# Kernel tuning notes

Hardware: AMD Instinct MI355X
Metric: run time of the kernel (lower is better)

## Reference

```python
import jax, jax.numpy as jnp
import numpy as np

WS = (8, 8)       # window size (wh, ww)
SS = (4, 4)       # shift size
NUM_HEADS = 8


def _relative_position_index(wh, ww):
    coords = np.stack(np.meshgrid(np.arange(wh), np.arange(ww), indexing='ij'))  # [2,wh,ww]
    cf = coords.reshape(2, -1)                                # [2, N]
    rel = (cf[:, :, None] - cf[:, None, :]).transpose(1, 2, 0)  # [N,N,2]
    rel[..., 0] += wh - 1
    rel[..., 1] += ww - 1
    rel[..., 0] *= 2 * ww - 1
    return rel.sum(-1).reshape(-1)                            # [N*N]


def _shift_attn_mask(H, W, wh, ww, sh, sw):
    img = np.zeros((H, W), dtype=np.float32)
    cnt = 0
    for hs in ((0, -wh), (-wh, -sh), (-sh, None)):
        for ws_ in ((0, -ww), (-ww, -sw), (-sw, None)):
            img[hs[0]:hs[1], ws_[0]:ws_[1]] = cnt
            cnt += 1
    m = img.reshape(H // wh, wh, W // ww, ww).transpose(0, 2, 1, 3).reshape(-1, wh * ww)  # [nW, N]
    diff = m[:, None, :] - m[:, :, None]                      # [nW, N, N]
    return np.where(diff != 0, -100.0, 0.0).astype(np.float32)


def setup_inputs() -> dict:
    key = jax.random.key(0)
    ks = jax.random.split(key, 6)
    B, H, W, C = 16, 128, 128, 256
    return {
        'x': jax.random.normal(ks[0], (B, H, W, C), jnp.float32),
        'qkv_weight': jax.random.normal(ks[1], (3 * C, C), jnp.float32) * 0.02,
        'qkv_bias': jax.random.normal(ks[2], (3 * C,), jnp.float32) * 0.02,
        'proj_weight': jax.random.normal(ks[3], (C, C), jnp.float32) * 0.02,
        'proj_bias': jax.random.normal(ks[4], (C,), jnp.float32) * 0.02,
        'rel_bias_table': jax.random.normal(ks[5], ((2 * WS[0] - 1) * (2 * WS[1] - 1), NUM_HEADS), jnp.float32) * 0.02,
    }


def reference(x, qkv_weight, qkv_bias, proj_weight, proj_bias, rel_bias_table):
    B, H, W, C = x.shape
    wh, ww = WS
    sh, sw = SS
    nh = NUM_HEADS
    hd = C // nh
    N = wh * ww
    nW = (H // wh) * (W // ww)

    # relative position bias [1, nh, N, N]
    rpi = _relative_position_index(wh, ww)
    bias = rel_bias_table[rpi].reshape(N, N, nh).transpose(2, 0, 1)[None]

    # shift (H, W divisible by window -> no padding needed)
    xs = jnp.roll(x, shift=(-sh, -sw), axis=(1, 2))
    # window partition -> [B*nW, N, C]
    xw = xs.reshape(B, H // wh, wh, W // ww, ww, C).transpose(0, 1, 3, 2, 4, 5).reshape(B * nW, N, C)

    qkv = xw @ qkv_weight.T + qkv_bias                        # [BnW, N, 3C]
    qkv = qkv.reshape(B * nW, N, 3, nh, hd).transpose(2, 0, 3, 1, 4)
    q, k, v = qkv[0], qkv[1], qkv[2]                          # [BnW, nh, N, hd]
    q = q * (hd ** -0.5)

    attn = jnp.einsum('whnd,whmd->whnm', q, k) + bias         # [BnW, nh, N, N]
    if sh + sw > 0:
        mask = jnp.asarray(_shift_attn_mask(H, W, wh, ww, sh, sw))  # [nW, N, N]
        attn = attn.reshape(B, nW, nh, N, N) + mask[None, :, None]
        attn = attn.reshape(B * nW, nh, N, N)
    attn = jax.nn.softmax(attn, axis=-1)

    out = jnp.einsum('whnm,whmd->whnd', attn, v)              # [BnW, nh, N, hd]
    out = out.transpose(0, 2, 1, 3).reshape(B * nW, N, C)
    out = out @ proj_weight.T + proj_bias

    # window reverse
    out = out.reshape(B, H // wh, W // ww, wh, ww, C).transpose(0, 1, 3, 2, 4, 5).reshape(B, H, W, C)
    out = jnp.roll(out, shift=(sh, sw), axis=(1, 2))
    return out
```

## Files before the change

### kernel.cpp

```cpp
#include <hip/hip_runtime.h>


typedef float f32x4 __attribute__((ext_vector_type(4)));
typedef __bf16 bf16x8 __attribute__((ext_vector_type(8)));
typedef unsigned short u16x4 __attribute__((ext_vector_type(4)));
typedef unsigned short u16x8 __attribute__((ext_vector_type(8)));

#define MFMA16(a, b, c) __builtin_amdgcn_mfma_f32_16x16x32_bf16((a), (b), (c), 0, 0, 0)

__device__ __forceinline__ unsigned short f2bf(float f) {
  union { float f; unsigned u; } v; v.f = f;
  unsigned r = v.u + 0x7FFFu + ((v.u >> 16) & 1u);
  return (unsigned short)(r >> 16);
}

__device__ __forceinline__ bf16x8 pack8(float4 f0, float4 f1) {
  union { u16x8 s; bf16x8 v; } u;
  u.s[0] = f2bf(f0.x); u.s[1] = f2bf(f0.y); u.s[2] = f2bf(f0.z); u.s[3] = f2bf(f0.w);
  u.s[4] = f2bf(f1.x); u.s[5] = f2bf(f1.y); u.s[6] = f2bf(f1.z); u.s[7] = f2bf(f1.w);
  return u.v;
}

__device__ __forceinline__ bf16x8 ld8u(const unsigned short* p) {
  union { unsigned long long q[2]; bf16x8 v; } u;
  u.q[0] = *(const unsigned long long*)(p);
  u.q[1] = *(const unsigned long long*)(p + 4);
  return u.v;
}

#define Q_OFF   0
#define K_OFF   18432
#define V_OFF   36864
#define TAB_OFF 55296
#define P_OFF   58912
#define SM_TOT  77344

__global__ void conv_weights(const float* __restrict__ qkvW, const float* __restrict__ projW,
                             unsigned short* __restrict__ wq, unsigned short* __restrict__ wp) {
  int i = blockIdx.x * 256 + threadIdx.x;
  if (i < 196608) wq[i] = f2bf(qkvW[i]);
  if (i < 65536)  wp[i] = f2bf(projW[i]);
}

template <bool PRE>
__global__ __launch_bounds__(256, 1) void swin_fused(
    const float* __restrict__ x,
    const float* __restrict__ qkvWf,
    const float* __restrict__ qkvB,
    const float* __restrict__ projWf,
    const float* __restrict__ projB,
    const float* __restrict__ relTab,
    const unsigned short* __restrict__ qkvWb,
    const unsigned short* __restrict__ projWb,
    float* __restrict__ out) {
  __shared__ unsigned short sm[SM_TOT];
  const f32x4 Z = {0.0f, 0.0f, 0.0f, 0.0f};

  const int tid = threadIdx.x;
  const int wv  = tid >> 6;
  const int lane = tid & 63;
  const int g  = lane >> 4;
  const int cl = lane & 15;
  const int blk = blockIdx.x;
  const int b  = blk >> 8;
  const int w  = blk & 255;
  const int wi = w >> 4, wj = w & 15;
  const bool er = (wi == 15), ec = (wj == 15);

  {
    float* t = (float*)(sm + TAB_OFF);
    for (int i = tid; i < 1800; i += 256) t[i] = relTab[i];
  }
  {
    unsigned short* X = sm + P_OFF;
    const float* xb = x + (size_t)b * (128 * 128 * 256);
#pragma unroll
    for (int it = 0; it < 8; ++it) {
      int idx = tid + it * 256;
      int t = idx >> 5, ch = idx & 31;
      int hh = (wi * 8 + (t >> 3) + 4) & 127;
      int ww = (wj * 8 + (t & 7) + 4) & 127;
      const float* src = xb + (((hh << 7) + ww) << 8) + ch * 8;
      float4 f0 = *(const float4*)src;
      float4 f1 = *(const float4*)(src + 4);
      u16x8 pk;
      pk[0] = f2bf(f0.x); pk[1] = f2bf(f0.y); pk[2] = f2bf(f0.z); pk[3] = f2bf(f0.w);
      pk[4] = f2bf(f1.x); pk[5] = f2bf(f1.y); pk[6] = f2bf(f1.z); pk[7] = f2bf(f1.w);
      *(u16x8*)(X + t * 256 + ((ch ^ (t & 7)) << 3)) = pk;
    }
  }
  __syncthreads();

  {
    const unsigned short* X = sm + P_OFF;
    for (int ct = wv * 12; ct < wv * 12 + 12; ++ct) {
      const int cb = ct << 4;
      bf16x8 bw[8];
#pragma unroll
      for (int ks = 0; ks < 8; ++ks) {
        const int off = (cb + cl) * 256 + ks * 32 + g * 8;
        if (PRE) {
          bw[ks] = *(const bf16x8*)(qkvWb + off);
        } else {
          float4 f0 = *(const float4*)(qkvWf + off);
          float4 f1 = *(const float4*)(qkvWf + off + 4);
          bw[ks] = pack8(f0, f1);
        }
      }
      f32x4 acc[4] = {Z, Z, Z, Z};
#pragma unroll
      for (int rt = 0; rt < 4; ++rt) {
        const int t = rt * 16 + cl;
        const unsigned short* xr = X + t * 256;
        const int t7 = t & 7;
#pragma unroll
        for (int ks = 0; ks < 8; ++ks) {
          bf16x8 a = *(const bf16x8*)(xr + (((ks * 4 + g) ^ t7) << 3));
          acc[rt] = MFMA16(a, bw[ks], acc[rt]);
        }
      }
      const int col = cb + cl;
      const float bias = qkvB[col];
      const int sel = col >> 8;
      const int hd_ = (col >> 5) & 7;
      const int dim = col & 31;
#pragma unroll
      for (int rt = 0; rt < 4; ++rt) {
#pragma unroll
        for (int rg = 0; rg < 4; ++rg) {
          const int t = rt * 16 + g * 4 + rg;
          float v = acc[rt][rg] + bias;
          if (sel == 0) {
            sm[Q_OFF + hd_ * 2304 + t * 36 + dim] = f2bf(v * 0.17677669529663687f);
          } else if (sel == 1) {
            sm[K_OFF + hd_ * 2304 + t * 36 + dim] = f2bf(v);
          } else {
            sm[V_OFF + (hd_ * 32 + dim) * 72 + t] = f2bf(v);
          }
        }
      }
    }
  }
  __syncthreads();

  {
    const float* tab = (const float*)(sm + TAB_OFF);
    unsigned short* P = sm + P_OFF + wv * 4608;
    float rsum[4];
#pragma unroll 1
    for (int hp = 0; hp < 2; ++hp) {
      const int h = wv * 2 + hp;
      const unsigned short* qh = sm + Q_OFF + h * 2304;
      const unsigned short* kh = sm + K_OFF + h * 2304;
      const unsigned short* vh = sm + V_OFF + h * (32 * 72);

      bf16x8 aq[4], ak[4];
#pragma unroll
      for (int qt = 0; qt < 4; ++qt) {
        aq[qt] = ld8u(qh + (qt * 16 + cl) * 36 + g * 8);
        ak[qt] = ld8u(kh + (qt * 16 + cl) * 36 + g * 8);
      }
      f32x4 s[4][4];
#pragma unroll
      for (int qt = 0; qt < 4; ++qt)
#pragma unroll
        for (int jt = 0; jt < 4; ++jt)
          s[qt][jt] = MFMA16(ak[jt], aq[qt], Z);

#pragma unroll
      for (int qt = 0; qt < 4; ++qt) {
        const int i = qt * 16 + cl;
        const int ri = i >> 3, ci = i & 7;
        const int ridi = (er ? ((ri < 4) ? 3 : 6) : 0) + (ec ? ((ci < 4) ? 1 : 2) : 0);
        float m = -1e30f;
#pragma unroll
        for (int jt = 0; jt < 4; ++jt) {
#pragma unroll
          for (int rg = 0; rg < 4; ++rg) {
            const int j = jt * 16 + g * 4 + rg;
            const int rj = j >> 3, cj = j & 7;
            const int ridj = (er ? ((rj < 4) ? 3 : 6) : 0) + (ec ? ((cj < 4) ? 1 : 2) : 0);
            float val = s[qt][jt][rg] + tab[((ri - rj + 7) * 15 + (ci - cj + 7)) * 8 + h];
            if (ridi != ridj) val -= 100.0f;
            s[qt][jt][rg] = val;
            m = fmaxf(m, val);
          }
        }
        m = fmaxf(m, __shfl_xor(m, 16));
        m = fmaxf(m, __shfl_xor(m, 32));
        float sum = 0.0f;
#pragma unroll
        for (int jt = 0; jt < 4; ++jt)
#pragma unroll
          for (int rg = 0; rg < 4; ++rg) {
            float e = __expf(s[qt][jt][rg] - m);
            s[qt][jt][rg] = e;
            sum += e;
          }
        sum += __shfl_xor(sum, 16);
        sum += __shfl_xor(sum, 32);
        rsum[qt] = 1.0f / sum;
      }

#pragma unroll
      for (int qt = 0; qt < 4; ++qt) {
        const int i = qt * 16 + cl;
#pragma unroll
        for (int jt = 0; jt < 4; ++jt) {
          u16x4 pk;
          pk[0] = f2bf(s[qt][jt][0]); pk[1] = f2bf(s[qt][jt][1]);
          pk[2] = f2bf(s[qt][jt][2]); pk[3] = f2bf(s[qt][jt][3]);
          *(u16x4*)(P + i * 72 + jt * 16 + g * 4) = pk;
        }
      }

      f32x4 o[2][4] = {{Z, Z, Z, Z}, {Z, Z, Z, Z}};
#pragma unroll
      for (int ks = 0; ks < 2; ++ks) {
        bf16x8 av[2], bp[4];
        av[0] = *(const bf16x8*)(vh + cl * 72 + ks * 32 + g * 8);
        av[1] = *(const bf16x8*)(vh + (16 + cl) * 72 + ks * 32 + g * 8);
#pragma unroll
        for (int qt = 0; qt < 4; ++qt)
          bp[qt] = *(const bf16x8*)(P + (qt * 16 + cl) * 72 + ks * 32 + g * 8);
#pragma unroll
        for (int dt = 0; dt < 2; ++dt)
#pragma unroll
          for (int qt = 0; qt < 4; ++qt)
            o[dt][qt] = MFMA16(av[dt], bp[qt], o[dt][qt]);
      }
#pragma unroll
      for (int dt = 0; dt < 2; ++dt)
#pragma unroll
        for (int qt = 0; qt < 4; ++qt) {
          u16x4 pk;
#pragma unroll
          for (int rg = 0; rg < 4; ++rg) pk[rg] = f2bf(o[dt][qt][rg] * rsum[qt]);
          const int t = qt * 16 + cl;
          *(u16x4*)(sm + Q_OFF + h * 2304 + t * 36 + dt * 16 + g * 4) = pk;
        }
    }
  }
  __syncthreads();

  {
    for (int ct = wv * 4; ct < wv * 4 + 4; ++ct) {
      const int cb = ct << 4;
      bf16x8 bw[8];
#pragma unroll
      for (int ks = 0; ks < 8; ++ks) {
        const int off = (cb + cl) * 256 + ks * 32 + g * 8;
        if (PRE) {
          bw[ks] = *(const bf16x8*)(projWb + off);
        } else {
          float4 f0 = *(const float4*)(projWf + off);
          float4 f1 = *(const float4*)(projWf + off + 4);
          bw[ks] = pack8(f0, f1);
        }
      }
      f32x4 acc[4] = {Z, Z, Z, Z};
#pragma unroll
      for (int rt = 0; rt < 4; ++rt) {
#pragma unroll
        for (int ks = 0; ks < 8; ++ks) {
          bf16x8 a = ld8u(sm + Q_OFF + ks * 2304 + (rt * 16 + cl) * 36 + g * 8);
          acc[rt] = MFMA16(a, bw[ks], acc[rt]);
        }
      }
      const int chn = cb + cl;
      const float pb = projB[chn];
#pragma unroll
      for (int rt = 0; rt < 4; ++rt) {
#pragma unroll
        for (int rg = 0; rg < 4; ++rg) {
          const int t = rt * 16 + g * 4 + rg;
          const int ho = (wi * 8 + (t >> 3) + 4) & 127;
          const int wo = (wj * 8 + (t & 7) + 4) & 127;
          out[((size_t)((b << 14) + (ho << 7) + wo) << 8) + chn] = acc[rt][rg] + pb;
        }
      }
    }
  }
}

extern "C" void kernel_launch(void* const* d_in, const int* in_sizes, int n_in,
                              void* d_out, int out_size, void* d_ws, size_t ws_size,
                              hipStream_t stream) {
  const float* x     = (const float*)d_in[0];
  const float* qkvW  = (const float*)d_in[1];
  const float* qkvB  = (const float*)d_in[2];
  const float* projW = (const float*)d_in[3];
  const float* projB = (const float*)d_in[4];
  const float* tab   = (const float*)d_in[5];
  float* out = (float*)d_out;

  const size_t need = (size_t)(196608 + 65536) * sizeof(unsigned short);
  if (ws_size >= need) {
    unsigned short* wq = (unsigned short*)d_ws;
    unsigned short* wp = wq + 196608;
    conv_weights<<<dim3(768), dim3(256), 0, stream>>>(qkvW, projW, wq, wp);
    swin_fused<true><<<dim3(4096), dim3(256), 0, stream>>>(
        x, qkvW, qkvB, projW, projB, tab, wq, wp, out);
  } else {
    swin_fused<false><<<dim3(4096), dim3(256), 0, stream>>>(
        x, qkvW, qkvB, projW, projB, tab, nullptr, nullptr, out);
  }
}
```

Measured before the change: 1.002 ms.

## Restructure fused Swin kernel per-head with smaller LDS and precomputed bias+mask

Each wave now computes Q, K and V for its own two heads and goes straight into attention from registers, using a small per-wave LDS scratch. This replaces the full-window Q/K/V staging in shared memory. LDS use drops from about 150KB to about 48KB, and launch bounds are raised to allow 3 blocks per CU. A prep kernel precomputes the relative-position bias plus shift mask for the four edge variants and folds the q scale into the bf16 qkv weights. The cost is more register pressure and a reworked, swizzled LDS layout, plus a global bias read per score tile.

```diff
diff --git a/kernel.cpp b/kernel.cpp
--- a/kernel.cpp
+++ b/kernel.cpp
@@ -7,6 +7,7 @@
 typedef unsigned short u16x8 __attribute__((ext_vector_type(8)));
 
 #define MFMA16(a, b, c) __builtin_amdgcn_mfma_f32_16x16x32_bf16((a), (b), (c), 0, 0, 0)
+#define QSCALE 0.17677669529663687f
 
 __device__ __forceinline__ unsigned short f2bf(float f) {
   union { float f; unsigned u; } v; v.f = f;
@@ -21,265 +22,294 @@
   return u.v;
 }
 
-__device__ __forceinline__ bf16x8 ld8u(const unsigned short* p) {
-  union { unsigned long long q[2]; bf16x8 v; } u;
-  u.q[0] = *(const unsigned long long*)(p);
-  u.q[1] = *(const unsigned long long*)(p + 4);
-  return u.v;
-}
-
-#define Q_OFF   0
-#define K_OFF   18432
-#define V_OFF   36864
-#define TAB_OFF 55296
-#define P_OFF   58912
-#define SM_TOT  77344
-
-__global__ void conv_weights(const float* __restrict__ qkvW, const float* __restrict__ projW,
-                             unsigned short* __restrict__ wq, unsigned short* __restrict__ wp) {
+__global__ void prep(const float* __restrict__ qkvW, const float* __restrict__ projW,
+                     const float* __restrict__ relTab,
+                     unsigned short* __restrict__ wq, unsigned short* __restrict__ wp,
+                     float* __restrict__ biasm) {
   int i = blockIdx.x * 256 + threadIdx.x;
-  if (i < 196608) wq[i] = f2bf(qkvW[i]);
-  if (i < 65536)  wp[i] = f2bf(projW[i]);
+  if (i < 196608) {
+    float v = qkvW[i];
+    if (i < 65536) v *= QSCALE;
+    wq[i] = f2bf(v);
+  }
+  if (i < 65536) wp[i] = f2bf(projW[i]);
+  if (i < 131072) {
+    int j = i & 63, ii = (i >> 6) & 63, h = (i >> 12) & 7, var = i >> 15;
+    int er = var >> 1, ec = var & 1;
+    int ri = ii >> 3, ci = ii & 7, rj = j >> 3, cj = j & 7;
+    int ridi = (er ? ((ri < 4) ? 3 : 6) : 0) + (ec ? ((ci < 4) ? 1 : 2) : 0);
+    int ridj = (er ? ((rj < 4) ? 3 : 6) : 0) + (ec ? ((cj < 4) ? 1 : 2) : 0);
+    float v = relTab[((ri - rj + 7) * 15 + (ci - cj + 7)) * 8 + h];
+    if (ridi != ridj) v -= 100.0f;
+    biasm[i] = v;
+  }
 }
 
 template <bool PRE>
-__global__ __launch_bounds__(256, 1) void swin_fused(
+__global__ __launch_bounds__(256, 3) void swin_fused(
     const float* __restrict__ x,
-    const float* __restrict__ qkvWf,
-    const float* __restrict__ qkvB,
-    const float* __restrict__ projWf,
-    const float* __restrict__ projB,
+    const float* __restrict__ qkvWf, const float* __restrict__ qkvB,
+    const float* __restrict__ projWf, const float* __restrict__ projB,
     const float* __restrict__ relTab,
     const unsigned short* __restrict__ qkvWb,
     const unsigned short* __restrict__ projWb,
+    const float* __restrict__ biasm,
     float* __restrict__ out) {
-  __shared__ unsigned short sm[SM_TOT];
+  __shared__ unsigned short sm[PRE ? 24576 : 28192];
   const f32x4 Z = {0.0f, 0.0f, 0.0f, 0.0f};
 
   const int tid = threadIdx.x;
-  const int wv  = tid >> 6;
-  const int lane = tid & 63;
-  const int g  = lane >> 4;
-  const int cl = lane & 15;
-  const int blk = blockIdx.x;
-  const int b  = blk >> 8;
-  const int w  = blk & 255;
-  const int wi = w >> 4, wj = w & 15;
+  const int wv = tid >> 6, lane = tid & 63, g = lane >> 4, cl = lane & 15;
+  const int blk = blockIdx.x, b = blk >> 8, w = blk & 255, wi = w >> 4, wj = w & 15;
   const bool er = (wi == 15), ec = (wj == 15);
+  const int var = (er ? 2 : 0) + (ec ? 1 : 0);
+
+  if (!PRE) {
+    float* t = (float*)(sm + 24576);
+    for (int i = tid; i < 1800; i += 256) t[i] = relTab[i];
+  }
 
   {
-    float* t = (float*)(sm + TAB_OFF);
-    for (int i = tid; i < 1800; i += 256) t[i] = relTab[i];
-  }
-  {
-    unsigned short* X = sm + P_OFF;
     const float* xb = x + (size_t)b * (128 * 128 * 256);
 #pragma unroll
     for (int it = 0; it < 8; ++it) {
-      int idx = tid + it * 256;
-      int t = idx >> 5, ch = idx & 31;
+      int idx = tid + it * 256, t = idx >> 5, ch = idx & 31;
       int hh = (wi * 8 + (t >> 3) + 4) & 127;
       int ww = (wj * 8 + (t & 7) + 4) & 127;
-      const float* src = xb + (((hh << 7) + ww) << 8) + ch * 8;
+      const float* src = xb + ((((hh << 7) + ww) << 8) + ch * 8);
       float4 f0 = *(const float4*)src;
       float4 f1 = *(const float4*)(src + 4);
-      u16x8 pk;
-      pk[0] = f2bf(f0.x); pk[1] = f2bf(f0.y); pk[2] = f2bf(f0.z); pk[3] = f2bf(f0.w);
-      pk[4] = f2bf(f1.x); pk[5] = f2bf(f1.y); pk[6] = f2bf(f1.z); pk[7] = f2bf(f1.w);
-      *(u16x8*)(X + t * 256 + ((ch ^ (t & 7)) << 3)) = pk;
+      union { u16x8 s; bf16x8 v; } pk;
+      pk.s[0] = f2bf(f0.x); pk.s[1] = f2bf(f0.y); pk.s[2] = f2bf(f0.z); pk.s[3] = f2bf(f0.w);
+      pk.s[4] = f2bf(f1.x); pk.s[5] = f2bf(f1.y); pk.s[6] = f2bf(f1.z); pk.s[7] = f2bf(f1.w);
+      *(u16x8*)(sm + ch * 512 + ((t ^ (2 * (ch & 3))) << 3)) = pk.s;
     }
   }
   __syncthreads();
 
-  {
-    const unsigned short* X = sm + P_OFF;
-    for (int ct = wv * 12; ct < wv * 12 + 12; ++ct) {
-      const int cb = ct << 4;
+  unsigned short* scr = sm + 16384 + wv * 2048;
+  const int hA = wv * 2, hB = hA + 1;
+
+  auto ldx = [&](int row, int c) -> bf16x8 {
+    return *(const bf16x8*)(sm + c * 512 + ((row ^ (2 * (c & 3))) << 3));
+  };
+  auto gemm32 = [&](int colbase, f32x4 (&acc)[2][4]) {
+#pragma unroll
+    for (int ct = 0; ct < 2; ++ct) {
+      const int col = colbase + ct * 16 + cl;
       bf16x8 bw[8];
 #pragma unroll
       for (int ks = 0; ks < 8; ++ks) {
-        const int off = (cb + cl) * 256 + ks * 32 + g * 8;
-        if (PRE) {
-          bw[ks] = *(const bf16x8*)(qkvWb + off);
-        } else {
-          float4 f0 = *(const float4*)(qkvWf + off);
-          float4 f1 = *(const float4*)(qkvWf + off + 4);
-          bw[ks] = pack8(f0, f1);
+        const int off = col * 256 + ks * 32 + g * 8;
+        if (PRE) bw[ks] = *(const bf16x8*)(qkvWb + off);
+        else {
+          float4 a = *(const float4*)(qkvWf + off);
+          float4 c2 = *(const float4*)(qkvWf + off + 4);
+          bw[ks] = pack8(a, c2);
         }
       }
-      f32x4 acc[4] = {Z, Z, Z, Z};
 #pragma unroll
       for (int rt = 0; rt < 4; ++rt) {
-        const int t = rt * 16 + cl;
-        const unsigned short* xr = X + t * 256;
-        const int t7 = t & 7;
-#pragma unroll
-        for (int ks = 0; ks < 8; ++ks) {
-          bf16x8 a = *(const bf16x8*)(xr + (((ks * 4 + g) ^ t7) << 3));
-          acc[rt] = MFMA16(a, bw[ks], acc[rt]);
+        acc[ct][rt] = Z;
+#pragma unroll
+        for (int ks = 0; ks < 8; ++ks)
+          acc[ct][rt] = MFMA16(ldx(rt * 16 + cl, ks * 4 + g), bw[ks], acc[ct][rt]);
+      }
+    }
+  };
+  auto epiQK = [&](f32x4 (&acc)[2][4], int colbase, bool isQ) {
+#pragma unroll
+    for (int ct = 0; ct < 2; ++ct) {
+      const int col = colbase + ct * 16 + cl;
+      float bs = qkvB[col]; if (isQ) bs *= QSCALE;
+      const int cQ = 2 * ct + (cl >> 3), Xr = 2 * (cQ & 3);
+#pragma unroll
+      for (int rt = 0; rt < 4; ++rt)
+#pragma unroll
+        for (int r = 0; r < 4; ++r) {
+          float v = acc[ct][rt][r];
+          if (!PRE && isQ) v *= QSCALE;
+          scr[cQ * 512 + (((rt * 16 + 4 * g + r) ^ Xr) << 3) + (cl & 7)] = f2bf(v + bs);
         }
-      }
-      const int col = cb + cl;
-      const float bias = qkvB[col];
-      const int sel = col >> 8;
-      const int hd_ = (col >> 5) & 7;
-      const int dim = col & 31;
+    }
+  };
+  auto ldQK = [&](int it) -> bf16x8 {
+    return *(const bf16x8*)(scr + g * 512 + (((it * 16 + cl) ^ (2 * g)) << 3));
+  };
+  auto epiV = [&](f32x4 (&acc)[2][4], int colbase) {
+#pragma unroll
+    for (int ct = 0; ct < 2; ++ct) {
+      const int col = colbase + ct * 16 + cl;
+      const float bs = qkvB[col];
 #pragma unroll
       for (int rt = 0; rt < 4; ++rt) {
-#pragma unroll
-        for (int rg = 0; rg < 4; ++rg) {
-          const int t = rt * 16 + g * 4 + rg;
-          float v = acc[rt][rg] + bias;
-          if (sel == 0) {
-            sm[Q_OFF + hd_ * 2304 + t * 36 + dim] = f2bf(v * 0.17677669529663687f);
-          } else if (sel == 1) {
-            sm[K_OFF + hd_ * 2304 + t * 36 + dim] = f2bf(v);
-          } else {
-            sm[V_OFF + (hd_ * 32 + dim) * 72 + t] = f2bf(v);
-          }
-        }
-      }
-    }
-  }
-  __syncthreads();
-
-  {
-    const float* tab = (const float*)(sm + TAB_OFF);
-    unsigned short* P = sm + P_OFF + wv * 4608;
-    float rsum[4];
-#pragma unroll 1
-    for (int hp = 0; hp < 2; ++hp) {
-      const int h = wv * 2 + hp;
-      const unsigned short* qh = sm + Q_OFF + h * 2304;
-      const unsigned short* kh = sm + K_OFF + h * 2304;
-      const unsigned short* vh = sm + V_OFF + h * (32 * 72);
-
-      bf16x8 aq[4], ak[4];
-#pragma unroll
-      for (int qt = 0; qt < 4; ++qt) {
-        aq[qt] = ld8u(qh + (qt * 16 + cl) * 36 + g * 8);
-        ak[qt] = ld8u(kh + (qt * 16 + cl) * 36 + g * 8);
-      }
-      f32x4 s[4][4];
-#pragma unroll
-      for (int qt = 0; qt < 4; ++qt)
-#pragma unroll
-        for (int jt = 0; jt < 4; ++jt)
-          s[qt][jt] = MFMA16(ak[jt], aq[qt], Z);
-
-#pragma unroll
-      for (int qt = 0; qt < 4; ++qt) {
-        const int i = qt * 16 + cl;
+        const int cV = 2 * rt + (g >> 1);
+        const int pos = (ct * 16 + cl) ^ (2 * (cV & 3));
+        u16x4 pk;
+#pragma unroll
+        for (int r = 0; r < 4; ++r) pk[r] = f2bf(acc[ct][rt][r] + bs);
+        *(u16x4*)(scr + cV * 256 + pos * 8 + 4 * (g & 1)) = pk;
+      }
+    }
+  };
+  auto ldV = [&](int ks, int dt) -> bf16x8 {
+    const int c = ks * 4 + g;
+    return *(const bf16x8*)(scr + c * 256 + (((dt * 16 + cl) ^ (2 * (c & 3))) << 3));
+  };
+  auto attnHead = [&](int h, bf16x8 (&aq)[4], bf16x8 (&ak)[4], bf16x8 (&bv)[2][2],
+                      f32x4 (&o)[4][2]) {
+    bf16x8 ap[4][2];
+#pragma unroll
+    for (int qt = 0; qt < 4; ++qt) {
+      f32x4 s4[4];
+#pragma unroll
+      for (int jt = 0; jt < 4; ++jt) s4[jt] = MFMA16(ak[jt], aq[qt], Z);
+      const int i = qt * 16 + cl;
+      if (PRE) {
+        const float* bp = biasm + (((var * 8 + h) * 64 + i) << 6) + g * 4;
+#pragma unroll
+        for (int jt = 0; jt < 4; ++jt) s4[jt] += *(const f32x4*)(bp + jt * 16);
+      } else {
+        const float* tab = (const float*)(sm + 24576);
         const int ri = i >> 3, ci = i & 7;
         const int ridi = (er ? ((ri < 4) ? 3 : 6) : 0) + (ec ? ((ci < 4) ? 1 : 2) : 0);
-        float m = -1e30f;
-#pragma unroll
-        for (int jt = 0; jt < 4; ++jt) {
-#pragma unroll
-          for (int rg = 0; rg < 4; ++rg) {
-            const int j = jt * 16 + g * 4 + rg;
-            const int rj = j >> 3, cj = j & 7;
+#pragma unroll
+        for (int jt = 0; jt < 4; ++jt)
+#pragma unroll
+          for (int r = 0; r < 4; ++r) {
+            const int j = jt * 16 + 4 * g + r, rj = j >> 3, cj = j & 7;
             const int ridj = (er ? ((rj < 4) ? 3 : 6) : 0) + (ec ? ((cj < 4) ? 1 : 2) : 0);
-            float val = s[qt][jt][rg] + tab[((ri - rj + 7) * 15 + (ci - cj + 7)) * 8 + h];
-            if (ridi != ridj) val -= 100.0f;
-            s[qt][jt][rg] = val;
-            m = fmaxf(m, val);
+            float v2 = s4[jt][r] + tab[((ri - rj + 7) * 15 + (ci - cj + 7)) * 8 + h];
+            if (ridi != ridj) v2 -= 100.0f;
+            s4[jt][r] = v2;
           }
+      }
+      float mx = -1e30f;
+#pragma unroll
+      for (int jt = 0; jt < 4; ++jt)
+#pragma unroll
+        for (int r = 0; r < 4; ++r) mx = fmaxf(mx, s4[jt][r]);
+      mx = fmaxf(mx, __shfl_xor(mx, 16));
+      mx = fmaxf(mx, __shfl_xor(mx, 32));
+      float sum = 0.0f;
+#pragma unroll
+      for (int jt = 0; jt < 4; ++jt)
+#pragma unroll
+        for (int r = 0; r < 4; ++r) {
+          float e = __expf(s4[jt][r] - mx);
+          s4[jt][r] = e; sum += e;
         }
-        m = fmaxf(m, __shfl_xor(m, 16));
-        m = fmaxf(m, __shfl_xor(m, 32));
-        float sum = 0.0f;
-#pragma unroll
-        for (int jt = 0; jt < 4; ++jt)
-#pragma unroll
-          for (int rg = 0; rg < 4; ++rg) {
-            float e = __expf(s[qt][jt][rg] - m);
-            s[qt][jt][rg] = e;
-            sum += e;
-          }
-        sum += __shfl_xor(sum, 16);
-        sum += __shfl_xor(sum, 32);
-        rsum[qt] = 1.0f / sum;
-      }
-
-#pragma unroll
-      for (int qt = 0; qt < 4; ++qt) {
-        const int i = qt * 16 + cl;
-#pragma unroll
-        for (int jt = 0; jt < 4; ++jt) {
-          u16x4 pk;
-          pk[0] = f2bf(s[qt][jt][0]); pk[1] = f2bf(s[qt][jt][1]);
-          pk[2] = f2bf(s[qt][jt][2]); pk[3] = f2bf(s[qt][jt][3]);
-          *(u16x4*)(P + i * 72 + jt * 16 + g * 4) = pk;
-        }
-      }
-
-      f32x4 o[2][4] = {{Z, Z, Z, Z}, {Z, Z, Z, Z}};
-#pragma unroll
-      for (int ks = 0; ks < 2; ++ks) {
-        bf16x8 av[2], bp[4];
-        av[0] = *(const bf16x8*)(vh + cl * 72 + ks * 32 + g * 8);
-        av[1] = *(const bf16x8*)(vh + (16 + cl) * 72 + ks * 32 + g * 8);
-#pragma unroll
-        for (int qt = 0; qt < 4; ++qt)
-          bp[qt] = *(const bf16x8*)(P + (qt * 16 + cl) * 72 + ks * 32 + g * 8);
-#pragma unroll
-        for (int dt = 0; dt < 2; ++dt)
-#pragma unroll
-          for (int qt = 0; qt < 4; ++qt)
-            o[dt][qt] = MFMA16(av[dt], bp[qt], o[dt][qt]);
-      }
-#pragma unroll
-      for (int dt = 0; dt < 2; ++dt)
-#pragma unroll
-        for (int qt = 0; qt < 4; ++qt) {
-          u16x4 pk;
-#pragma unroll
-          for (int rg = 0; rg < 4; ++rg) pk[rg] = f2bf(o[dt][qt][rg] * rsum[qt]);
-          const int t = qt * 16 + cl;
-          *(u16x4*)(sm + Q_OFF + h * 2304 + t * 36 + dt * 16 + g * 4) = pk;
-        }
-    }
+      sum += __shfl_xor(sum, 16);
+      sum += __shfl_xor(sum, 32);
+      const float rs = 1.0f / sum;
+#pragma unroll
+      for (int jt = 0; jt < 4; ++jt) {
+        const int cP = 2 * jt + (g >> 1);
+        const int pos = cl ^ (2 * (cP & 3));
+        u16x4 pk;
+#pragma unroll
+        for (int r = 0; r < 4; ++r) pk[r] = f2bf(s4[jt][r] * rs);
+        *(u16x4*)(scr + cP * 128 + pos * 8 + 4 * (g & 1)) = pk;
+      }
+#pragma unroll
+      for (int ks = 0; ks < 2; ++ks)
+        ap[qt][ks] = *(const bf16x8*)(scr + (ks * 4 + g) * 128 + ((cl ^ (2 * g)) << 3));
+    }
+#pragma unroll
+    for (int it = 0; it < 4; ++it)
+#pragma unroll
+      for (int dt = 0; dt < 2; ++dt) {
+        o[it][dt] = Z;
+#pragma unroll
+        for (int ks = 0; ks < 2; ++ks)
+          o[it][dt] = MFMA16(ap[it][ks], bv[ks][dt], o[it][dt]);
+      }
+  };
+  auto writeO = [&](int h, f32x4 (&o)[4][2]) {
+#pragma unroll
+    for (int it = 0; it < 4; ++it)
+#pragma unroll
+      for (int dt = 0; dt < 2; ++dt) {
+        const int d = h * 32 + dt * 16 + cl;
+        const int cA = d >> 3, Xr = 2 * (cA & 3);
+#pragma unroll
+        for (int r = 0; r < 4; ++r)
+          sm[cA * 512 + (((it * 16 + 4 * g + r) ^ Xr) << 3) + (d & 7)] = f2bf(o[it][dt][r]);
+      }
+  };
+
+  bf16x8 aqA[4], akA[4], bvA[2][2], aqB[4], akB[4], bvB[2][2];
+  {
+    f32x4 acc[2][4];
+    gemm32(hA * 32, acc);        epiQK(acc, hA * 32, true);
+#pragma unroll
+    for (int i2 = 0; i2 < 4; ++i2) aqA[i2] = ldQK(i2);
+    gemm32(256 + hA * 32, acc);  epiQK(acc, 256 + hA * 32, false);
+#pragma unroll
+    for (int i2 = 0; i2 < 4; ++i2) akA[i2] = ldQK(i2);
+    gemm32(512 + hA * 32, acc);  epiV(acc, 512 + hA * 32);
+#pragma unroll
+    for (int ks = 0; ks < 2; ++ks)
+#pragma unroll
+      for (int dt = 0; dt < 2; ++dt) bvA[ks][dt] = ldV(ks, dt);
+    gemm32(hB * 32, acc);        epiQK(acc, hB * 32, true);
+#pragma unroll
+    for (int i2 = 0; i2 < 4; ++i2) aqB[i2] = ldQK(i2);
+    gemm32(256 + hB * 32, acc);  epiQK(acc, 256 + hB * 32, false);
+#pragma unroll
+    for (int i2 = 0; i2 < 4; ++i2) akB[i2] = ldQK(i2);
+  }
+  f32x4 oA[4][2];
+  attnHead(hA, aqA, akA, bvA, oA);
+  {
+    f32x4 acc[2][4];
+    gemm32(512 + hB * 32, acc);  epiV(acc, 512 + hB * 32);
+#pragma unroll
+    for (int ks = 0; ks < 2; ++ks)
+#pragma unroll
+      for (int dt = 0; dt < 2; ++dt) bvB[ks][dt] = ldV(ks, dt);
   }
   __syncthreads();
-
+  writeO(hA, oA);
   {
-    for (int ct = wv * 4; ct < wv * 4 + 4; ++ct) {
-      const int cb = ct << 4;
-      bf16x8 bw[8];
-#pragma unroll
-      for (int ks = 0; ks < 8; ++ks) {
-        const int off = (cb + cl) * 256 + ks * 32 + g * 8;
-        if (PRE) {
-          bw[ks] = *(const bf16x8*)(projWb + off);
-        } else {
-          float4 f0 = *(const float4*)(projWf + off);
-          float4 f1 = *(const float4*)(projWf + off + 4);
-          bw[ks] = pack8(f0, f1);
-        }
-      }
-      f32x4 acc[4] = {Z, Z, Z, Z};
-#pragma unroll
-      for (int rt = 0; rt < 4; ++rt) {
-#pragma unroll
-        for (int ks = 0; ks < 8; ++ks) {
-          bf16x8 a = ld8u(sm + Q_OFF + ks * 2304 + (rt * 16 + cl) * 36 + g * 8);
-          acc[rt] = MFMA16(a, bw[ks], acc[rt]);
-        }
-      }
-      const int chn = cb + cl;
-      const float pb = projB[chn];
-#pragma unroll
-      for (int rt = 0; rt < 4; ++rt) {
-#pragma unroll
-        for (int rg = 0; rg < 4; ++rg) {
-          const int t = rt * 16 + g * 4 + rg;
-          const int ho = (wi * 8 + (t >> 3) + 4) & 127;
-          const int wo = (wj * 8 + (t & 7) + 4) & 127;
-          out[((size_t)((b << 14) + (ho << 7) + wo) << 8) + chn] = acc[rt][rg] + pb;
-        }
-      }
-    }
+    f32x4 oB[4][2];
+    attnHead(hB, aqB, akB, bvB, oB);
+    writeO(hB, oB);
+  }
+  __syncthreads();
+
+#pragma unroll 1
+  for (int ct = wv * 4; ct < wv * 4 + 4; ++ct) {
+    const int col = ct * 16 + cl;
+    bf16x8 bw[8];
+#pragma unroll
+    for (int ks = 0; ks < 8; ++ks) {
+      const int off = col * 256 + ks * 32 + g * 8;
+      if (PRE) bw[ks] = *(const bf16x8*)(projWb + off);
+      else {
+        float4 a = *(const float4*)(projWf + off);
+        float4 c2 = *(const float4*)(projWf + off + 4);
+        bw[ks] = pack8(a, c2);
+      }
+    }
+    f32x4 acc[4];
+#pragma unroll
+    for (int rt = 0; rt < 4; ++rt) {
+      acc[rt] = Z;
+#pragma unroll
+      for (int ks = 0; ks < 8; ++ks)
+        acc[rt] = MFMA16(ldx(rt * 16 + cl, ks * 4 + g), bw[ks], acc[rt]);
+    }
+    const float pb = projB[col];
+#pragma unroll
+    for (int rt = 0; rt < 4; ++rt)
+#pragma unroll
+      for (int r = 0; r < 4; ++r) {
+        const int t = rt * 16 + 4 * g + r;
+        const int ho = (wi * 8 + (t >> 3) + 4) & 127;
+        const int wo = (wj * 8 + (t & 7) + 4) & 127;
+        out[((size_t)((b << 14) + (ho << 7) + wo) << 8) + col] = acc[rt][r] + pb;
+      }
   }
 }
 
@@ -294,15 +324,17 @@
   const float* tab   = (const float*)d_in[5];
   float* out = (float*)d_out;
 
-  const size_t need = (size_t)(196608 + 65536) * sizeof(unsigned short);
+  const size_t needW = (size_t)(196608 + 65536) * sizeof(unsigned short);
+  const size_t need  = needW + (size_t)131072 * sizeof(float);
   if (ws_size >= need) {
     unsigned short* wq = (unsigned short*)d_ws;
     unsigned short* wp = wq + 196608;
-    conv_weights<<<dim3(768), dim3(256), 0, stream>>>(qkvW, projW, wq, wp);
+    float* biasm = (float*)((char*)d_ws + needW);
+    prep<<<dim3(768), dim3(256), 0, stream>>>(qkvW, projW, tab, wq, wp, biasm);
     swin_fused<true><<<dim3(4096), dim3(256), 0, stream>>>(
-        x, qkvW, qkvB, projW, projB, tab, wq, wp, out);
+        x, qkvW, qkvB, projW, projB, tab, wq, wp, biasm, out);
   } else {
     swin_fused<false><<<dim3(4096), dim3(256), 0, stream>>>(
-        x, qkvW, qkvB, projW, projB, tab, nullptr, nullptr, out);
-  }
-}
+        x, qkvW, qkvB, projW, projB, tab, nullptr, nullptr, nullptr, out);
+  }
+}
```

After: 817.4 us. 1.23x faster.
